# Kernel tuning notes

Measured on AMD Instinct MI355X. Metric: run time of the kernel, lower is better.

Reference implementation:

```python
import jax, jax.numpy as jnp
import numpy as np

NA, NB = 40000, 40000
D_IN, D_OUT, H, C = 256, 256, 8, 32  # C = D_OUT // H
E = 400000
N_MP = 3


def setup_inputs() -> dict:
    key = jax.random.key(0)
    ks = jax.random.split(key, 16)
    s = 1.0 / np.sqrt(D_IN)
    inp = {
        "x_A": jax.random.normal(ks[0], (NA, D_IN), jnp.float32),
        "x_B": jax.random.normal(ks[1], (NB, D_IN), jnp.float32),
        "edge_ab": jax.random.randint(ks[2], (2, E), 0, NB, jnp.int32),  # src in A, dst in B
        "edge_ba": jax.random.randint(ks[3], (2, E), 0, NA, jnp.int32),  # src in B, dst in A
        "edge_aa": jax.random.randint(ks[4], (2, E), 0, NA, jnp.int32),  # src in A, dst in A
        "W_A": jax.random.normal(ks[5], (D_IN, D_OUT), jnp.float32) * s,
        "b_A": jnp.zeros((D_OUT,), jnp.float32),
        "W_B": jax.random.normal(ks[6], (D_IN, D_OUT), jnp.float32) * s,
        "b_B": jnp.zeros((D_OUT,), jnp.float32),
        "attn_l": jax.random.normal(ks[7], (N_MP, H, C), jnp.float32) * 0.1,
        "attn_r": jax.random.normal(ks[8], (N_MP, H, C), jnp.float32) * 0.1,
        "rel_l_A": jax.random.normal(ks[9], (H, C), jnp.float32) * 0.1,
        "rel_r_A": jax.random.normal(ks[10], (H, C), jnp.float32) * 0.1,
        "rel_l_B": jax.random.normal(ks[11], (H, C), jnp.float32) * 0.1,
        "rel_r_B": jax.random.normal(ks[12], (H, C), jnp.float32) * 0.1,
    }
    return inp


def _leaky(x):
    return jax.nn.leaky_relu(x, negative_slope=0.2)


def _gat_relation(h_src, edge, a_l, a_r, n_dst):
    """GAT-style edge attention + segment softmax + scatter-add.
    h_src: [N_src,H,C], edge: [2,E], a_l: [N_src,H], a_r: [N_dst,H]."""
    src, dst = edge[0], edge[1]
    e = _leaky(a_l[src] + a_r[dst])                      # [E,H]
    m = jax.ops.segment_max(e, dst, num_segments=n_dst)  # [N_dst,H]
    ex = jnp.exp(e - m[dst])
    denom = jax.ops.segment_sum(ex, dst, num_segments=n_dst)
    alpha = ex / denom[dst]                              # softmax over in-neighbors
    msg = h_src[src] * alpha[:, :, None]                 # [E,H,C]
    return jax.ops.segment_sum(msg, dst, num_segments=n_dst)  # [N_dst,H,C]


def _beta_combine(h, rel_embs, rel_l, rel_r):
    """Relation-level attention (get_beta_weights) + weighted sum.
    h: [N,H,C], rel_embs: [N,H,R,C]."""
    bl = (h * rel_l).sum(-1)                                 # [N,H]
    br = (rel_embs * rel_r[None, :, None, :]).sum(-1)        # [N,H,R]
    beta = jax.nn.softmax(_leaky(bl[:, :, None] + br), axis=2)
    out = (rel_embs * beta[..., None]).sum(2)                # [N,H,C]
    return out.reshape(out.shape[0], H * C)


def reference(x_A, x_B, edge_ab, edge_ba, edge_aa, W_A, b_A, W_B, b_B,
              attn_l, attn_r, rel_l_A, rel_r_A, rel_l_B, rel_r_B):
    nA, nB = x_A.shape[0], x_B.shape[0]
    h_A = (x_A @ W_A + b_A).reshape(nA, H, C)
    h_B = (x_B @ W_B + b_B).reshape(nB, H, C)

    # per-metapath node attention scalars (get_alphas)
    # metapath 0: A->B, 1: B->A, 2: A->A
    al0 = (h_A * attn_l[0]).sum(-1); ar0 = (h_B * attn_r[0]).sum(-1)
    al1 = (h_B * attn_l[1]).sum(-1); ar1 = (h_A * attn_r[1]).sum(-1)
    al2 = (h_A * attn_l[2]).sum(-1); ar2 = (h_A * attn_r[2]).sum(-1)

    # aggregate per tail relation (agg_relation_neighbors); last slot = self
    rel_ba = _gat_relation(h_B, edge_ba, al1, ar1, nA)
    rel_aa = _gat_relation(h_A, edge_aa, al2, ar2, nA)
    emb_A = jnp.stack([rel_ba, rel_aa, h_A], axis=2)         # [NA,H,3,C]

    rel_ab = _gat_relation(h_A, edge_ab, al0, ar0, nB)
    emb_B = jnp.stack([rel_ab, h_B], axis=2)                 # [NB,H,2,C]

    out_A = jax.nn.relu(_beta_combine(h_A, emb_A, rel_l_A, rel_r_A))
    out_B = jax.nn.relu(_beta_combine(h_B, emb_B, rel_l_B, rel_r_B))
    return jnp.concatenate([out_A, out_B], axis=0)           # [NA+NB, D_OUT]
```

## Files before the change

### kernel.cpp

```cpp
#include <hip/hip_runtime.h>
#include <math.h>

#define NAn 40000
#define NBn 40000
#define DIN 256
#define DOUT 256
#define NH 8
#define NC 32
#define NE 400000
#define CAP 64

typedef __attribute__((ext_vector_type(8))) short short8;
typedef __attribute__((ext_vector_type(4))) float floatx4;

__device__ __forceinline__ float leaky(float x) { return x > 0.f ? x : 0.2f * x; }
__device__ __forceinline__ float dot4(float4 a, float4 b) {
  return a.x * b.x + a.y * b.y + a.z * b.z + a.w * b.w;
}
__device__ __forceinline__ unsigned bf16_rne_bits(float x) {
  unsigned u = __float_as_uint(x);
  unsigned r = u + 0x7fffu + ((u >> 16) & 1u);
  return r & 0xffff0000u;
}
__device__ __forceinline__ float4 bf4(uint2 u) {
  float4 f;
  f.x = __uint_as_float(u.x << 16);
  f.y = __uint_as_float(u.x & 0xffff0000u);
  f.z = __uint_as_float(u.y << 16);
  f.w = __uint_as_float(u.y & 0xffff0000u);
  return f;
}
__device__ __forceinline__ void bf8(uint4 u, float* f) {
  f[0] = __uint_as_float(u.x << 16);
  f[1] = __uint_as_float(u.x & 0xffff0000u);
  f[2] = __uint_as_float(u.y << 16);
  f[3] = __uint_as_float(u.y & 0xffff0000u);
  f[4] = __uint_as_float(u.z << 16);
  f[5] = __uint_as_float(u.z & 0xffff0000u);
  f[6] = __uint_as_float(u.w << 16);
  f[7] = __uint_as_float(u.w & 0xffff0000u);
}

__global__ void wswz(const float* __restrict__ WA, const float* __restrict__ WB,
                     short8* __restrict__ hiA, short8* __restrict__ hiB) {
  int t = blockIdx.x * blockDim.x + threadIdx.x;
  const float* W;
  short8* hi;
  if (t < 8192) {
    W = WA; hi = hiA;
  } else {
    t -= 8192;
    if (t >= 8192) return;
    W = WB; hi = hiB;
  }
  int kt = t >> 10, nt = (t >> 6) & 15, l = t & 63;
  int n = nt * 16 + (l & 15);
  int kb = kt * 32 + (l >> 4) * 8;
  short8 h8;
#pragma unroll
  for (int j = 0; j < 8; ++j) {
    float w = W[(size_t)(kb + j) * DOUT + n];
    h8[j] = (short)(bf16_rne_bits(w) >> 16);
  }
  hi[t] = h8;
}

__global__ __launch_bounds__(256) void gemm_mfma(
    const float* __restrict__ XA, const float* __restrict__ XB,
    const short8* __restrict__ WAhi, const short8* __restrict__ WBhi,
    const float* __restrict__ bA, const float* __restrict__ bB,
    unsigned* __restrict__ HAbf, unsigned* __restrict__ HBbf) {
  __shared__ short8 bfrag[2][1024];
  int blk = blockIdx.x;
  const float* X;
  const short8* Wh;
  const float* bias;
  unsigned* Hbf;
  if (blk < NAn / 64) {
    X = XA; Wh = WAhi; bias = bA; Hbf = HAbf;
  } else {
    blk -= NAn / 64;
    X = XB; Wh = WBhi; bias = bB; Hbf = HBbf;
  }
  const int tid = threadIdx.x;
  const int lane = tid & 63, wave = tid >> 6;
  const int row0 = blk * 64 + wave * 16;
  const int col16 = lane & 15, quad = lane >> 4;

  floatx4 acc[16];
#pragma unroll
  for (int i = 0; i < 16; ++i) acc[i] = (floatx4){0.f, 0.f, 0.f, 0.f};

  const float4* xp = (const float4*)(X + (size_t)(row0 + col16) * DIN) + quad * 2;

  uint4 pre[4];
  const uint4* wsrc = (const uint4*)Wh;
#pragma unroll
  for (int c = 0; c < 4; ++c) pre[c] = wsrc[c * 256 + tid];
  {
    uint4* d = (uint4*)&bfrag[0][0];
#pragma unroll
    for (int c = 0; c < 4; ++c) d[c * 256 + tid] = pre[c];
  }
  __syncthreads();

  for (int kt = 0; kt < 8; ++kt) {
    if (kt < 7) {
      const uint4* s = wsrc + (size_t)(kt + 1) * 1024;
#pragma unroll
      for (int c = 0; c < 4; ++c) pre[c] = s[c * 256 + tid];
    }
    float4 x0 = xp[kt * 8];
    float4 x1 = xp[kt * 8 + 1];
    float xv[8] = {x0.x, x0.y, x0.z, x0.w, x1.x, x1.y, x1.z, x1.w};
    short8 ahi, alo;
#pragma unroll
    for (int j = 0; j < 8; ++j) {
      unsigned hb = bf16_rne_bits(xv[j]);
      ahi[j] = (short)(hb >> 16);
      float rem = xv[j] - __uint_as_float(hb);
      alo[j] = (short)(bf16_rne_bits(rem) >> 16);
    }
    const short8* bp = &bfrag[kt & 1][0];
#pragma unroll
    for (int nt = 0; nt < 16; ++nt) {
      short8 bv = bp[nt * 64 + lane];
      acc[nt] = __builtin_amdgcn_mfma_f32_16x16x32_bf16(ahi, bv, acc[nt], 0, 0, 0);
      acc[nt] = __builtin_amdgcn_mfma_f32_16x16x32_bf16(alo, bv, acc[nt], 0, 0, 0);
    }
    if (kt < 7) {
      uint4* d = (uint4*)&bfrag[(kt + 1) & 1][0];
#pragma unroll
      for (int c = 0; c < 4; ++c) d[c * 256 + tid] = pre[c];
    }
    __syncthreads();
  }
#pragma unroll
  for (int nt = 0; nt < 16; ++nt) {
    float bcol = bias[nt * 16 + col16];
#pragma unroll
    for (int r = 0; r < 4; ++r) {
      int row = row0 + quad * 4 + r;
      float v = acc[nt][r] + bcol;
      float vp = __shfl_xor(v, 1);
      if ((lane & 1) == 0) {
        unsigned p = (bf16_rne_bits(v) >> 16) | bf16_rne_bits(vp);
        Hbf[(size_t)row * 128 + nt * 8 + (col16 >> 1)] = p;
      }
    }
  }
}

__global__ void alphas(const uint2* __restrict__ hAbf, const uint2* __restrict__ hBbf,
                       const float* __restrict__ attn_l, const float* __restrict__ attn_r,
                       float* __restrict__ al0, float* __restrict__ ar1,
                       float* __restrict__ al2, float* __restrict__ ar2,
                       float* __restrict__ ar0, float* __restrict__ al1) {
  int idx = blockIdx.x * blockDim.x + threadIdx.x;
  if (idx >= (NAn + NBn) * NH) return;
  bool isA = idx < NAn * NH;
  int k = isA ? idx : idx - NAn * NH;
  int head = k & 7;
  const uint2* h8 = (isA ? hAbf : hBbf) + (size_t)k * 8;
  if (isA) {
    const float4* l0 = (const float4*)(attn_l + 0 * DOUT + head * NC);
    const float4* r1 = (const float4*)(attn_r + 1 * DOUT + head * NC);
    const float4* l2 = (const float4*)(attn_l + 2 * DOUT + head * NC);
    const float4* r2 = (const float4*)(attn_r + 2 * DOUT + head * NC);
    float s0 = 0, s1 = 0, s2 = 0, s3 = 0;
#pragma unroll
    for (int q = 0; q < 8; ++q) {
      float4 hv = bf4(h8[q]);
      s0 += dot4(hv, l0[q]);
      s1 += dot4(hv, r1[q]);
      s2 += dot4(hv, l2[q]);
      s3 += dot4(hv, r2[q]);
    }
    al0[k] = s0;
    ar1[k] = s1;
    al2[k] = s2;
    ar2[k] = s3;
  } else {
    const float4* r0 = (const float4*)(attn_r + 0 * DOUT + head * NC);
    const float4* l1 = (const float4*)(attn_l + 1 * DOUT + head * NC);
    float s0 = 0, s1 = 0;
#pragma unroll
    for (int q = 0; q < 8; ++q) {
      float4 hv = bf4(h8[q]);
      s0 += dot4(hv, r0[q]);
      s1 += dot4(hv, l1[q]);
    }
    ar0[k] = s0;
    al1[k] = s1;
  }
}

__global__ void build_csr3(const int* __restrict__ e_ba, const int* __restrict__ e_aa,
                           const int* __restrict__ e_ab, int* __restrict__ cnt_ba,
                           int* __restrict__ cnt_aa, int* __restrict__ cnt_ab,
                           int* __restrict__ sl_ba, int* __restrict__ sl_aa,
                           int* __restrict__ sl_ab) {
  int i = blockIdx.x * blockDim.x + threadIdx.x;
  if (i >= 3 * NE) return;
  const int* e;
  int* cnt;
  int* sl;
  int k = i;
  if (i < NE) {
    e = e_ba; cnt = cnt_ba; sl = sl_ba;
  } else if (i < 2 * NE) {
    e = e_aa; cnt = cnt_aa; sl = sl_aa; k = i - NE;
  } else {
    e = e_ab; cnt = cnt_ab; sl = sl_ab; k = i - 2 * NE;
  }
  int src = e[k];
  int dst = e[NE + k];
  int pos = atomicAdd(&cnt[dst], 1);
  if (pos < CAP) sl[(size_t)dst * CAP + pos] = src;
}

__device__ __forceinline__ void gat2(int dst, int wave, int lane, int h, int sub, int head,
                                     const int* __restrict__ cnt,
                                     const int* __restrict__ slots,
                                     const float* __restrict__ al,
                                     const float* __restrict__ ar,
                                     const uint4* __restrict__ hbf,
                                     int lds_slot[4][64], float lds_ex[4][512],
                                     float acc[8]) {
#pragma unroll
  for (int k = 0; k < 8; ++k) acc[k] = 0.f;
  int deg = cnt[dst];
  if (deg > CAP) deg = CAP;
  if (deg == 0) return;
  __threadfence_block();
  if (lane < deg) {
    int s = slots[(size_t)dst * CAP + lane];
    lds_slot[wave][lane] = s;
    float4 a0 = *(const float4*)(al + (size_t)s * 8);
    float4 a1 = *(const float4*)(al + (size_t)s * 8 + 4);
    float4 r0 = *(const float4*)(ar + (size_t)dst * 8);
    float4 r1 = *(const float4*)(ar + (size_t)dst * 8 + 4);
    float* exq = &lds_ex[wave][lane * 8];
    exq[0] = __expf(leaky(a0.x + r0.x));
    exq[1] = __expf(leaky(a0.y + r0.y));
    exq[2] = __expf(leaky(a0.z + r0.z));
    exq[3] = __expf(leaky(a0.w + r0.w));
    exq[4] = __expf(leaky(a1.x + r1.x));
    exq[5] = __expf(leaky(a1.y + r1.y));
    exq[6] = __expf(leaky(a1.z + r1.z));
    exq[7] = __expf(leaky(a1.w + r1.w));
  }
  __threadfence_block();
  float den = 0.f;
  int iters = (deg + 1) >> 1;
  for (int it = 0; it < iters; ++it) {
    int j = it * 2 + h;
    if (j < deg) {
      int sj = lds_slot[wave][j];
      float w = lds_ex[wave][j * 8 + head];
      uint4 u = hbf[(size_t)sj * 32 + sub];
      den += w;
      float f[8];
      bf8(u, f);
#pragma unroll
      for (int k = 0; k < 8; ++k) acc[k] += w * f[k];
    }
  }
#pragma unroll
  for (int k = 0; k < 8; ++k) acc[k] += __shfl_xor(acc[k], 32);
  den += __shfl_xor(den, 32);
  float inv = 1.f / den;
#pragma unroll
  for (int k = 0; k < 8; ++k) acc[k] *= inv;
}

__global__ __launch_bounds__(256) void agg_combine(
    const int* __restrict__ cnt_ba, const int* __restrict__ sl_ba,
    const float* __restrict__ al1, const float* __restrict__ ar1,
    const int* __restrict__ cnt_aa, const int* __restrict__ sl_aa,
    const float* __restrict__ al2, const float* __restrict__ ar2,
    const int* __restrict__ cnt_ab, const int* __restrict__ sl_ab,
    const float* __restrict__ al0, const float* __restrict__ ar0,
    const uint4* __restrict__ hAbf, const uint4* __restrict__ hBbf,
    const float* __restrict__ rlA, const float* __restrict__ rrA,
    const float* __restrict__ rlB, const float* __restrict__ rrB,
    float* __restrict__ outp) {
  __shared__ int lds_slot[4][64];
  __shared__ float lds_ex[4][512];
  int wave = threadIdx.x >> 6, lane = threadIdx.x & 63;
  int h = lane >> 5, sub = lane & 31, head = sub >> 2;
  bool isA = blockIdx.x < (NAn / 4);
  int dst = (isA ? blockIdx.x : blockIdx.x - NAn / 4) * 4 + wave;
  float m0[8], hv[8], o[8];
  if (isA) {
    float m1[8];
    gat2(dst, wave, lane, h, sub, head, cnt_ba, sl_ba, al1, ar1, hBbf, lds_slot, lds_ex, m0);
    gat2(dst, wave, lane, h, sub, head, cnt_aa, sl_aa, al2, ar2, hAbf, lds_slot, lds_ex, m1);
    uint4 us = hAbf[(size_t)dst * 32 + sub];
    bf8(us, hv);
    const float4* rl4 = (const float4*)rlA;
    const float4* rr4 = (const float4*)rrA;
    float4 rl0 = rl4[sub * 2], rl1 = rl4[sub * 2 + 1];
    float4 rr0 = rr4[sub * 2], rr1 = rr4[sub * 2 + 1];
    float rl8[8] = {rl0.x, rl0.y, rl0.z, rl0.w, rl1.x, rl1.y, rl1.z, rl1.w};
    float rr8[8] = {rr0.x, rr0.y, rr0.z, rr0.w, rr1.x, rr1.y, rr1.z, rr1.w};
    float pbl = 0, p0 = 0, p1 = 0, p2 = 0;
#pragma unroll
    for (int k = 0; k < 8; ++k) {
      pbl += hv[k] * rl8[k];
      p0 += m0[k] * rr8[k];
      p1 += m1[k] * rr8[k];
      p2 += hv[k] * rr8[k];
    }
#pragma unroll
    for (int d = 1; d < 4; d <<= 1) {
      pbl += __shfl_xor(pbl, d);
      p0 += __shfl_xor(p0, d);
      p1 += __shfl_xor(p1, d);
      p2 += __shfl_xor(p2, d);
    }
    float b0 = leaky(pbl + p0), b1 = leaky(pbl + p1), b2 = leaky(pbl + p2);
    float mx = fmaxf(b0, fmaxf(b1, b2));
    float w0 = __expf(b0 - mx), w1 = __expf(b1 - mx), w2 = __expf(b2 - mx);
    float inv = 1.f / (w0 + w1 + w2);
    w0 *= inv; w1 *= inv; w2 *= inv;
#pragma unroll
    for (int k = 0; k < 8; ++k)
      o[k] = fmaxf(0.f, m0[k] * w0 + m1[k] * w1 + hv[k] * w2);
  } else {
    gat2(dst, wave, lane, h, sub, head, cnt_ab, sl_ab, al0, ar0, hAbf, lds_slot, lds_ex, m0);
    uint4 us = hBbf[(size_t)dst * 32 + sub];
    bf8(us, hv);
    const float4* rl4 = (const float4*)rlB;
    const float4* rr4 = (const float4*)rrB;
    float4 rl0 = rl4[sub * 2], rl1 = rl4[sub * 2 + 1];
    float4 rr0 = rr4[sub * 2], rr1 = rr4[sub * 2 + 1];
    float rl8[8] = {rl0.x, rl0.y, rl0.z, rl0.w, rl1.x, rl1.y, rl1.z, rl1.w};
    float rr8[8] = {rr0.x, rr0.y, rr0.z, rr0.w, rr1.x, rr1.y, rr1.z, rr1.w};
    float pbl = 0, p0 = 0, p1 = 0;
#pragma unroll
    for (int k = 0; k < 8; ++k) {
      pbl += hv[k] * rl8[k];
      p0 += m0[k] * rr8[k];
      p1 += hv[k] * rr8[k];
    }
#pragma unroll
    for (int d = 1; d < 4; d <<= 1) {
      pbl += __shfl_xor(pbl, d);
      p0 += __shfl_xor(p0, d);
      p1 += __shfl_xor(p1, d);
    }
    float b0 = leaky(pbl + p0), b1 = leaky(pbl + p1);
    float mx = fmaxf(b0, b1);
    float w0 = __expf(b0 - mx), w1 = __expf(b1 - mx);
    float inv = 1.f / (w0 + w1);
    w0 *= inv; w1 *= inv;
#pragma unroll
    for (int k = 0; k < 8; ++k) o[k] = fmaxf(0.f, m0[k] * w0 + hv[k] * w1);
  }
  float* orow = outp + (size_t)(isA ? dst : NAn + dst) * DOUT + sub * 8;
  if (h == 0) {
    *(float4*)orow = (float4){o[0], o[1], o[2], o[3]};
    *(float4*)(orow + 4) = (float4){o[4], o[5], o[6], o[7]};
  }
}

extern "C" void kernel_launch(void* const* d_in, const int* in_sizes, int n_in, void* d_out,
                              int out_size, void* d_ws, size_t ws_size, hipStream_t stream) {
  const float* xA = (const float*)d_in[0];
  const float* xB = (const float*)d_in[1];
  const int* e_ab = (const int*)d_in[2];
  const int* e_ba = (const int*)d_in[3];
  const int* e_aa = (const int*)d_in[4];
  const float* WA = (const float*)d_in[5];
  const float* bA = (const float*)d_in[6];
  const float* WB = (const float*)d_in[7];
  const float* bB = (const float*)d_in[8];
  const float* attn_l = (const float*)d_in[9];
  const float* attn_r = (const float*)d_in[10];
  const float* rlA = (const float*)d_in[11];
  const float* rrA = (const float*)d_in[12];
  const float* rlB = (const float*)d_in[13];
  const float* rrB = (const float*)d_in[14];
  float* out = (float*)d_out;

  char* p = (char*)d_ws;
  auto alloc = [&](size_t bytes) -> char* {
    char* r = p;
    p += (bytes + 255) & ~(size_t)255;
    return r;
  };
  unsigned* hAbf = (unsigned*)alloc((size_t)NAn * DOUT * 2);
  unsigned* hBbf = (unsigned*)alloc((size_t)NBn * DOUT * 2);
  float* al0 = (float*)alloc((size_t)NAn * NH * 4);
  float* ar1 = (float*)alloc((size_t)NAn * NH * 4);
  float* al2 = (float*)alloc((size_t)NAn * NH * 4);
  float* ar2 = (float*)alloc((size_t)NAn * NH * 4);
  float* ar0 = (float*)alloc((size_t)NBn * NH * 4);
  float* al1 = (float*)alloc((size_t)NBn * NH * 4);
  short8* WAhi = (short8*)alloc((size_t)8192 * 16);
  short8* WBhi = (short8*)alloc((size_t)8192 * 16);
  int* cnts = (int*)alloc((size_t)3 * NAn * 4);
  int* cnt_ba = cnts;
  int* cnt_aa = cnts + NAn;
  int* cnt_ab = cnts + 2 * NAn;
  int* slots_ba = (int*)alloc((size_t)NAn * CAP * 4);
  int* slots_aa = (int*)alloc((size_t)NAn * CAP * 4);
  int* slots_ab = (int*)alloc((size_t)NBn * CAP * 4);

  hipMemsetAsync(cnts, 0, (size_t)3 * NAn * 4, stream);

  wswz<<<64, 256, 0, stream>>>(WA, WB, WAhi, WBhi);
  build_csr3<<<(3 * NE + 255) / 256, 256, 0, stream>>>(e_ba, e_aa, e_ab, cnt_ba, cnt_aa,
                                                       cnt_ab, slots_ba, slots_aa, slots_ab);
  gemm_mfma<<<(NAn + NBn) / 64, 256, 0, stream>>>(xA, xB, WAhi, WBhi, bA, bB, hAbf, hBbf);
  alphas<<<((NAn + NBn) * NH + 255) / 256, 256, 0, stream>>>(
      (const uint2*)hAbf, (const uint2*)hBbf, attn_l, attn_r, al0, ar1, al2, ar2, ar0, al1);
  agg_combine<<<(NAn + NBn) / 4, 256, 0, stream>>>(
      cnt_ba, slots_ba, al1, ar1, cnt_aa, slots_aa, al2, ar2, cnt_ab, slots_ab, al0, ar0,
      (const uint4*)hAbf, (const uint4*)hBbf, rlA, rrA, rlB, rrB, out);
}
```

Baseline: 433.2 us.

## Split edge gather four ways with software prefetch and fold counter reset into swizzle

The aggregation kernel now has each wave process four edges at a time, with 16 lanes per edge each loading two 16-byte chunks. The next edge's row is prefetched while the current one accumulates, and setup for both relations is done up front with a single fence. This aims to raise memory-level parallelism in the gather-bound aggregation, and a launch-bounds occupancy hint is added. The separate memset of the degree counters is folded into the weight-swizzle kernel to drop one launch. The costs are more registers for the doubled accumulators and more cross-lane reductions.

```diff
diff --git a/kernel.cpp b/kernel.cpp
--- a/kernel.cpp
+++ b/kernel.cpp
@@ -42,18 +42,21 @@
 }
 
 __global__ void wswz(const float* __restrict__ WA, const float* __restrict__ WB,
-                     short8* __restrict__ hiA, short8* __restrict__ hiB) {
+                     short8* __restrict__ hiA, short8* __restrict__ hiB,
+                     int* __restrict__ cnts) {
   int t = blockIdx.x * blockDim.x + threadIdx.x;
+  for (int i = t; i < 3 * NAn; i += 16384) cnts[i] = 0;
   const float* W;
   short8* hi;
-  if (t < 8192) {
+  int tt = t;
+  if (tt < 8192) {
     W = WA; hi = hiA;
   } else {
-    t -= 8192;
-    if (t >= 8192) return;
+    tt -= 8192;
+    if (tt >= 8192) return;
     W = WB; hi = hiB;
   }
-  int kt = t >> 10, nt = (t >> 6) & 15, l = t & 63;
+  int kt = tt >> 10, nt = (tt >> 6) & 15, l = tt & 63;
   int n = nt * 16 + (l & 15);
   int kb = kt * 32 + (l >> 4) * 8;
   short8 h8;
@@ -62,7 +65,7 @@
     float w = W[(size_t)(kb + j) * DOUT + n];
     h8[j] = (short)(bf16_rne_bits(w) >> 16);
   }
-  hi[t] = h8;
+  hi[tt] = h8;
 }
 
 __global__ __launch_bounds__(256) void gemm_mfma(
@@ -219,62 +222,77 @@
   if (pos < CAP) sl[(size_t)dst * CAP + pos] = src;
 }
 
-__device__ __forceinline__ void gat2(int dst, int wave, int lane, int h, int sub, int head,
-                                     const int* __restrict__ cnt,
-                                     const int* __restrict__ slots,
-                                     const float* __restrict__ al,
-                                     const float* __restrict__ ar,
-                                     const uint4* __restrict__ hbf,
-                                     int lds_slot[4][64], float lds_ex[4][512],
-                                     float acc[8]) {
-#pragma unroll
-  for (int k = 0; k < 8; ++k) acc[k] = 0.f;
+__device__ __forceinline__ int setup_rel(int dst, int wave, int lane, int ridx,
+                                         const int* __restrict__ cnt,
+                                         const int* __restrict__ slots,
+                                         const float* __restrict__ al,
+                                         const float* __restrict__ ar,
+                                         int lds_slot[4][2][64],
+                                         float lds_ex[4][2][512]) {
   int deg = cnt[dst];
   if (deg > CAP) deg = CAP;
-  if (deg == 0) return;
-  __threadfence_block();
   if (lane < deg) {
     int s = slots[(size_t)dst * CAP + lane];
-    lds_slot[wave][lane] = s;
+    lds_slot[wave][ridx][lane] = s;
     float4 a0 = *(const float4*)(al + (size_t)s * 8);
     float4 a1 = *(const float4*)(al + (size_t)s * 8 + 4);
     float4 r0 = *(const float4*)(ar + (size_t)dst * 8);
     float4 r1 = *(const float4*)(ar + (size_t)dst * 8 + 4);
-    float* exq = &lds_ex[wave][lane * 8];
-    exq[0] = __expf(leaky(a0.x + r0.x));
-    exq[1] = __expf(leaky(a0.y + r0.y));
-    exq[2] = __expf(leaky(a0.z + r0.z));
-    exq[3] = __expf(leaky(a0.w + r0.w));
-    exq[4] = __expf(leaky(a1.x + r1.x));
-    exq[5] = __expf(leaky(a1.y + r1.y));
-    exq[6] = __expf(leaky(a1.z + r1.z));
-    exq[7] = __expf(leaky(a1.w + r1.w));
-  }
-  __threadfence_block();
-  float den = 0.f;
-  int iters = (deg + 1) >> 1;
-  for (int it = 0; it < iters; ++it) {
-    int j = it * 2 + h;
-    if (j < deg) {
-      int sj = lds_slot[wave][j];
-      float w = lds_ex[wave][j * 8 + head];
-      uint4 u = hbf[(size_t)sj * 32 + sub];
-      den += w;
-      float f[8];
-      bf8(u, f);
-#pragma unroll
-      for (int k = 0; k < 8; ++k) acc[k] += w * f[k];
-    }
-  }
-#pragma unroll
-  for (int k = 0; k < 8; ++k) acc[k] += __shfl_xor(acc[k], 32);
-  den += __shfl_xor(den, 32);
-  float inv = 1.f / den;
-#pragma unroll
-  for (int k = 0; k < 8; ++k) acc[k] *= inv;
-}
-
-__global__ __launch_bounds__(256) void agg_combine(
+    float4 e0, e1;
+    e0.x = __expf(leaky(a0.x + r0.x));
+    e0.y = __expf(leaky(a0.y + r0.y));
+    e0.z = __expf(leaky(a0.z + r0.z));
+    e0.w = __expf(leaky(a0.w + r0.w));
+    e1.x = __expf(leaky(a1.x + r1.x));
+    e1.y = __expf(leaky(a1.y + r1.y));
+    e1.z = __expf(leaky(a1.z + r1.z));
+    e1.w = __expf(leaky(a1.w + r1.w));
+    *(float4*)&lds_ex[wave][ridx][lane * 8] = e0;
+    *(float4*)&lds_ex[wave][ridx][lane * 8 + 4] = e1;
+  }
+  return deg;
+}
+
+__device__ __forceinline__ void edges4(int deg, int wave, int ridx, int h4, int hd0,
+                                       int s16, const uint4* __restrict__ hbf,
+                                       int lds_slot[4][2][64], float lds_ex[4][2][512],
+                                       float acc0[8], float acc1[8], float& den0,
+                                       float& den1) {
+  int j = h4;
+  if (j >= deg) return;
+  int sj = lds_slot[wave][ridx][j];
+  float w0 = lds_ex[wave][ridx][j * 8 + hd0];
+  float w1 = lds_ex[wave][ridx][j * 8 + hd0 + 4];
+  const uint4* bp = hbf + (size_t)sj * 32;
+  uint4 u0 = bp[s16];
+  uint4 u1 = bp[s16 + 16];
+  while (true) {
+    uint4 cu0 = u0, cu1 = u1;
+    float cw0 = w0, cw1 = w1;
+    int jn = j + 4;
+    if (jn < deg) {
+      int sn = lds_slot[wave][ridx][jn];
+      w0 = lds_ex[wave][ridx][jn * 8 + hd0];
+      w1 = lds_ex[wave][ridx][jn * 8 + hd0 + 4];
+      const uint4* bn = hbf + (size_t)sn * 32;
+      u0 = bn[s16];
+      u1 = bn[s16 + 16];
+    }
+    den0 += cw0;
+    den1 += cw1;
+    float f0[8], f1[8];
+    bf8(cu0, f0);
+    bf8(cu1, f1);
+#pragma unroll
+    for (int k = 0; k < 8; ++k) acc0[k] += cw0 * f0[k];
+#pragma unroll
+    for (int k = 0; k < 8; ++k) acc1[k] += cw1 * f1[k];
+    j = jn;
+    if (j >= deg) break;
+  }
+}
+
+__global__ __launch_bounds__(256, 4) void agg_combine(
     const int* __restrict__ cnt_ba, const int* __restrict__ sl_ba,
     const float* __restrict__ al1, const float* __restrict__ ar1,
     const int* __restrict__ cnt_aa, const int* __restrict__ sl_aa,
@@ -285,83 +303,166 @@
     const float* __restrict__ rlA, const float* __restrict__ rrA,
     const float* __restrict__ rlB, const float* __restrict__ rrB,
     float* __restrict__ outp) {
-  __shared__ int lds_slot[4][64];
-  __shared__ float lds_ex[4][512];
+  __shared__ int lds_slot[4][2][64];
+  __shared__ float lds_ex[4][2][512];
   int wave = threadIdx.x >> 6, lane = threadIdx.x & 63;
-  int h = lane >> 5, sub = lane & 31, head = sub >> 2;
+  int h4 = lane >> 4, s16 = lane & 15;
+  int hd0 = s16 >> 2;
+  int c0 = s16, c1 = s16 + 16;
   bool isA = blockIdx.x < (NAn / 4);
   int dst = (isA ? blockIdx.x : blockIdx.x - NAn / 4) * 4 + wave;
-  float m0[8], hv[8], o[8];
+
   if (isA) {
-    float m1[8];
-    gat2(dst, wave, lane, h, sub, head, cnt_ba, sl_ba, al1, ar1, hBbf, lds_slot, lds_ex, m0);
-    gat2(dst, wave, lane, h, sub, head, cnt_aa, sl_aa, al2, ar2, hAbf, lds_slot, lds_ex, m1);
-    uint4 us = hAbf[(size_t)dst * 32 + sub];
-    bf8(us, hv);
+    int deg0 = setup_rel(dst, wave, lane, 0, cnt_ba, sl_ba, al1, ar1, lds_slot, lds_ex);
+    int deg1 = setup_rel(dst, wave, lane, 1, cnt_aa, sl_aa, al2, ar2, lds_slot, lds_ex);
+    uint4 us0 = hAbf[(size_t)dst * 32 + c0];
+    uint4 us1 = hAbf[(size_t)dst * 32 + c1];
+    __threadfence_block();
+    float m00[8], m01[8], m10[8], m11[8];
+    float den00 = 0.f, den01 = 0.f, den10 = 0.f, den11 = 0.f;
+#pragma unroll
+    for (int k = 0; k < 8; ++k) { m00[k] = 0.f; m01[k] = 0.f; m10[k] = 0.f; m11[k] = 0.f; }
+    edges4(deg0, wave, 0, h4, hd0, s16, hBbf, lds_slot, lds_ex, m00, m01, den00, den01);
+    edges4(deg1, wave, 1, h4, hd0, s16, hAbf, lds_slot, lds_ex, m10, m11, den10, den11);
+#pragma unroll
+    for (int k = 0; k < 8; ++k) {
+      m00[k] += __shfl_xor(m00[k], 16); m00[k] += __shfl_xor(m00[k], 32);
+      m01[k] += __shfl_xor(m01[k], 16); m01[k] += __shfl_xor(m01[k], 32);
+      m10[k] += __shfl_xor(m10[k], 16); m10[k] += __shfl_xor(m10[k], 32);
+      m11[k] += __shfl_xor(m11[k], 16); m11[k] += __shfl_xor(m11[k], 32);
+    }
+    den00 += __shfl_xor(den00, 16); den00 += __shfl_xor(den00, 32);
+    den01 += __shfl_xor(den01, 16); den01 += __shfl_xor(den01, 32);
+    den10 += __shfl_xor(den10, 16); den10 += __shfl_xor(den10, 32);
+    den11 += __shfl_xor(den11, 16); den11 += __shfl_xor(den11, 32);
+    if (deg0 > 0) {
+      float i0 = 1.f / den00, i1 = 1.f / den01;
+#pragma unroll
+      for (int k = 0; k < 8; ++k) { m00[k] *= i0; m01[k] *= i1; }
+    }
+    if (deg1 > 0) {
+      float i0 = 1.f / den10, i1 = 1.f / den11;
+#pragma unroll
+      for (int k = 0; k < 8; ++k) { m10[k] *= i0; m11[k] *= i1; }
+    }
+    float hv0[8], hv1[8];
+    bf8(us0, hv0);
+    bf8(us1, hv1);
     const float4* rl4 = (const float4*)rlA;
     const float4* rr4 = (const float4*)rrA;
-    float4 rl0 = rl4[sub * 2], rl1 = rl4[sub * 2 + 1];
-    float4 rr0 = rr4[sub * 2], rr1 = rr4[sub * 2 + 1];
-    float rl8[8] = {rl0.x, rl0.y, rl0.z, rl0.w, rl1.x, rl1.y, rl1.z, rl1.w};
-    float rr8[8] = {rr0.x, rr0.y, rr0.z, rr0.w, rr1.x, rr1.y, rr1.z, rr1.w};
-    float pbl = 0, p0 = 0, p1 = 0, p2 = 0;
+    float4 la = rl4[c0 * 2], lb = rl4[c0 * 2 + 1], lc = rl4[c1 * 2], ld = rl4[c1 * 2 + 1];
+    float4 ra = rr4[c0 * 2], rb = rr4[c0 * 2 + 1], rc = rr4[c1 * 2], rd = rr4[c1 * 2 + 1];
+    float rl0[8] = {la.x, la.y, la.z, la.w, lb.x, lb.y, lb.z, lb.w};
+    float rl1[8] = {lc.x, lc.y, lc.z, lc.w, ld.x, ld.y, ld.z, ld.w};
+    float rr0[8] = {ra.x, ra.y, ra.z, ra.w, rb.x, rb.y, rb.z, rb.w};
+    float rr1[8] = {rc.x, rc.y, rc.z, rc.w, rd.x, rd.y, rd.z, rd.w};
+    float pbl0 = 0, pbl1 = 0, q00 = 0, q01 = 0, q10 = 0, q11 = 0, q20 = 0, q21 = 0;
 #pragma unroll
     for (int k = 0; k < 8; ++k) {
-      pbl += hv[k] * rl8[k];
-      p0 += m0[k] * rr8[k];
-      p1 += m1[k] * rr8[k];
-      p2 += hv[k] * rr8[k];
+      pbl0 += hv0[k] * rl0[k]; pbl1 += hv1[k] * rl1[k];
+      q00 += m00[k] * rr0[k];  q01 += m01[k] * rr1[k];
+      q10 += m10[k] * rr0[k];  q11 += m11[k] * rr1[k];
+      q20 += hv0[k] * rr0[k];  q21 += hv1[k] * rr1[k];
     }
 #pragma unroll
     for (int d = 1; d < 4; d <<= 1) {
-      pbl += __shfl_xor(pbl, d);
-      p0 += __shfl_xor(p0, d);
-      p1 += __shfl_xor(p1, d);
-      p2 += __shfl_xor(p2, d);
-    }
-    float b0 = leaky(pbl + p0), b1 = leaky(pbl + p1), b2 = leaky(pbl + p2);
+      pbl0 += __shfl_xor(pbl0, d); pbl1 += __shfl_xor(pbl1, d);
+      q00 += __shfl_xor(q00, d);   q01 += __shfl_xor(q01, d);
+      q10 += __shfl_xor(q10, d);   q11 += __shfl_xor(q11, d);
+      q20 += __shfl_xor(q20, d);   q21 += __shfl_xor(q21, d);
+    }
+    float b0 = leaky(pbl0 + q00), b1 = leaky(pbl0 + q10), b2 = leaky(pbl0 + q20);
     float mx = fmaxf(b0, fmaxf(b1, b2));
     float w0 = __expf(b0 - mx), w1 = __expf(b1 - mx), w2 = __expf(b2 - mx);
     float inv = 1.f / (w0 + w1 + w2);
     w0 *= inv; w1 *= inv; w2 *= inv;
-#pragma unroll
-    for (int k = 0; k < 8; ++k)
-      o[k] = fmaxf(0.f, m0[k] * w0 + m1[k] * w1 + hv[k] * w2);
+    float d0 = leaky(pbl1 + q01), d1 = leaky(pbl1 + q11), d2 = leaky(pbl1 + q21);
+    float mx1 = fmaxf(d0, fmaxf(d1, d2));
+    float v0 = __expf(d0 - mx1), v1 = __expf(d1 - mx1), v2 = __expf(d2 - mx1);
+    float inv1 = 1.f / (v0 + v1 + v2);
+    v0 *= inv1; v1 *= inv1; v2 *= inv1;
+    if (h4 == 0) {
+      float o0[8], o1[8];
+#pragma unroll
+      for (int k = 0; k < 8; ++k) {
+        o0[k] = fmaxf(0.f, m00[k] * w0 + m10[k] * w1 + hv0[k] * w2);
+        o1[k] = fmaxf(0.f, m01[k] * v0 + m11[k] * v1 + hv1[k] * v2);
+      }
+      float* orow = outp + (size_t)dst * DOUT;
+      *(float4*)(orow + c0 * 8) = (float4){o0[0], o0[1], o0[2], o0[3]};
+      *(float4*)(orow + c0 * 8 + 4) = (float4){o0[4], o0[5], o0[6], o0[7]};
+      *(float4*)(orow + c1 * 8) = (float4){o1[0], o1[1], o1[2], o1[3]};
+      *(float4*)(orow + c1 * 8 + 4) = (float4){o1[4], o1[5], o1[6], o1[7]};
+    }
   } else {
-    gat2(dst, wave, lane, h, sub, head, cnt_ab, sl_ab, al0, ar0, hAbf, lds_slot, lds_ex, m0);
-    uint4 us = hBbf[(size_t)dst * 32 + sub];
-    bf8(us, hv);
+    int deg = setup_rel(dst, wave, lane, 0, cnt_ab, sl_ab, al0, ar0, lds_slot, lds_ex);
+    uint4 us0 = hBbf[(size_t)dst * 32 + c0];
+    uint4 us1 = hBbf[(size_t)dst * 32 + c1];
+    __threadfence_block();
+    float m00[8], m01[8];
+    float den00 = 0.f, den01 = 0.f;
+#pragma unroll
+    for (int k = 0; k < 8; ++k) { m00[k] = 0.f; m01[k] = 0.f; }
+    edges4(deg, wave, 0, h4, hd0, s16, hAbf, lds_slot, lds_ex, m00, m01, den00, den01);
+#pragma unroll
+    for (int k = 0; k < 8; ++k) {
+      m00[k] += __shfl_xor(m00[k], 16); m00[k] += __shfl_xor(m00[k], 32);
+      m01[k] += __shfl_xor(m01[k], 16); m01[k] += __shfl_xor(m01[k], 32);
+    }
+    den00 += __shfl_xor(den00, 16); den00 += __shfl_xor(den00, 32);
+    den01 += __shfl_xor(den01, 16); den01 += __shfl_xor(den01, 32);
+    if (deg > 0) {
+      float i0 = 1.f / den00, i1 = 1.f / den01;
+#pragma unroll
+      for (int k = 0; k < 8; ++k) { m00[k] *= i0; m01[k] *= i1; }
+    }
+    float hv0[8], hv1[8];
+    bf8(us0, hv0);
+    bf8(us1, hv1);
     const float4* rl4 = (const float4*)rlB;
     const float4* rr4 = (const float4*)rrB;
-    float4 rl0 = rl4[sub * 2], rl1 = rl4[sub * 2 + 1];
-    float4 rr0 = rr4[sub * 2], rr1 = rr4[sub * 2 + 1];
-    float rl8[8] = {rl0.x, rl0.y, rl0.z, rl0.w, rl1.x, rl1.y, rl1.z, rl1.w};
-    float rr8[8] = {rr0.x, rr0.y, rr0.z, rr0.w, rr1.x, rr1.y, rr1.z, rr1.w};
-    float pbl = 0, p0 = 0, p1 = 0;
+    float4 la = rl4[c0 * 2], lb = rl4[c0 * 2 + 1], lc = rl4[c1 * 2], ld = rl4[c1 * 2 + 1];
+    float4 ra = rr4[c0 * 2], rb = rr4[c0 * 2 + 1], rc = rr4[c1 * 2], rd = rr4[c1 * 2 + 1];
+    float rl0[8] = {la.x, la.y, la.z, la.w, lb.x, lb.y, lb.z, lb.w};
+    float rl1[8] = {lc.x, lc.y, lc.z, lc.w, ld.x, ld.y, ld.z, ld.w};
+    float rr0[8] = {ra.x, ra.y, ra.z, ra.w, rb.x, rb.y, rb.z, rb.w};
+    float rr1[8] = {rc.x, rc.y, rc.z, rc.w, rd.x, rd.y, rd.z, rd.w};
+    float pbl0 = 0, pbl1 = 0, q00 = 0, q01 = 0, q20 = 0, q21 = 0;
 #pragma unroll
     for (int k = 0; k < 8; ++k) {
-      pbl += hv[k] * rl8[k];
-      p0 += m0[k] * rr8[k];
-      p1 += hv[k] * rr8[k];
+      pbl0 += hv0[k] * rl0[k]; pbl1 += hv1[k] * rl1[k];
+      q00 += m00[k] * rr0[k];  q01 += m01[k] * rr1[k];
+      q20 += hv0[k] * rr0[k];  q21 += hv1[k] * rr1[k];
     }
 #pragma unroll
     for (int d = 1; d < 4; d <<= 1) {
-      pbl += __shfl_xor(pbl, d);
-      p0 += __shfl_xor(p0, d);
-      p1 += __shfl_xor(p1, d);
-    }
-    float b0 = leaky(pbl + p0), b1 = leaky(pbl + p1);
+      pbl0 += __shfl_xor(pbl0, d); pbl1 += __shfl_xor(pbl1, d);
+      q00 += __shfl_xor(q00, d);   q01 += __shfl_xor(q01, d);
+      q20 += __shfl_xor(q20, d);   q21 += __shfl_xor(q21, d);
+    }
+    float b0 = leaky(pbl0 + q00), b1 = leaky(pbl0 + q20);
     float mx = fmaxf(b0, b1);
     float w0 = __expf(b0 - mx), w1 = __expf(b1 - mx);
     float inv = 1.f / (w0 + w1);
     w0 *= inv; w1 *= inv;
-#pragma unroll
-    for (int k = 0; k < 8; ++k) o[k] = fmaxf(0.f, m0[k] * w0 + hv[k] * w1);
-  }
-  float* orow = outp + (size_t)(isA ? dst : NAn + dst) * DOUT + sub * 8;
-  if (h == 0) {
-    *(float4*)orow = (float4){o[0], o[1], o[2], o[3]};
-    *(float4*)(orow + 4) = (float4){o[4], o[5], o[6], o[7]};
+    float d0 = leaky(pbl1 + q01), d1 = leaky(pbl1 + q21);
+    float mx1 = fmaxf(d0, d1);
+    float v0 = __expf(d0 - mx1), v1 = __expf(d1 - mx1);
+    float inv1 = 1.f / (v0 + v1);
+    v0 *= inv1; v1 *= inv1;
+    if (h4 == 0) {
+      float o0[8], o1[8];
+#pragma unroll
+      for (int k = 0; k < 8; ++k) {
+        o0[k] = fmaxf(0.f, m00[k] * w0 + hv0[k] * w1);
+        o1[k] = fmaxf(0.f, m01[k] * v0 + hv1[k] * v1);
+      }
+      float* orow = outp + (size_t)(NAn + dst) * DOUT;
+      *(float4*)(orow + c0 * 8) = (float4){o0[0], o0[1], o0[2], o0[3]};
+      *(float4*)(orow + c0 * 8 + 4) = (float4){o0[4], o0[5], o0[6], o0[7]};
+      *(float4*)(orow + c1 * 8) = (float4){o1[0], o1[1], o1[2], o1[3]};
+      *(float4*)(orow + c1 * 8 + 4) = (float4){o1[4], o1[5], o1[6], o1[7]};
+    }
   }
 }
 
@@ -408,9 +509,7 @@
   int* slots_aa = (int*)alloc((size_t)NAn * CAP * 4);
   int* slots_ab = (int*)alloc((size_t)NBn * CAP * 4);
 
-  hipMemsetAsync(cnts, 0, (size_t)3 * NAn * 4, stream);
-
-  wswz<<<64, 256, 0, stream>>>(WA, WB, WAhi, WBhi);
+  wswz<<<64, 256, 0, stream>>>(WA, WB, WAhi, WBhi, cnts);
   build_csr3<<<(3 * NE + 255) / 256, 256, 0, stream>>>(e_ba, e_aa, e_ab, cnt_ba, cnt_aa,
                                                        cnt_ab, slots_ba, slots_aa, slots_ab);
   gemm_mfma<<<(NAn + NBn) / 64, 256, 0, stream>>>(xA, xB, WAhi, WBhi, bA, bB, hAbf, hBbf);
```

Result: slower. 475.0 us (+9.7%).

## Fuse attention-scalar computation into GEMM epilogue and fold counter memset into weight swizzle

Applied to the files above, without the earlier changes.

The GEMM epilogue now also writes the bf16 outputs to LDS, then computes the per-node, per-head attention dot products there. This removes the separate alphas kernel and its re-read of the projected features from global memory. The count-array memset moves into the weight-swizzle kernel to save one launch, and the CSR build uses nontemporal loads and stores for edges and slots. The cost is extra epilogue work and LDS traffic in the GEMM.

```diff
diff --git a/kernel.cpp b/kernel.cpp
--- a/kernel.cpp
+++ b/kernel.cpp
@@ -14,21 +14,10 @@
 typedef __attribute__((ext_vector_type(4))) float floatx4;
 
 __device__ __forceinline__ float leaky(float x) { return x > 0.f ? x : 0.2f * x; }
-__device__ __forceinline__ float dot4(float4 a, float4 b) {
-  return a.x * b.x + a.y * b.y + a.z * b.z + a.w * b.w;
-}
 __device__ __forceinline__ unsigned bf16_rne_bits(float x) {
   unsigned u = __float_as_uint(x);
   unsigned r = u + 0x7fffu + ((u >> 16) & 1u);
   return r & 0xffff0000u;
-}
-__device__ __forceinline__ float4 bf4(uint2 u) {
-  float4 f;
-  f.x = __uint_as_float(u.x << 16);
-  f.y = __uint_as_float(u.x & 0xffff0000u);
-  f.z = __uint_as_float(u.y << 16);
-  f.w = __uint_as_float(u.y & 0xffff0000u);
-  return f;
 }
 __device__ __forceinline__ void bf8(uint4 u, float* f) {
   f[0] = __uint_as_float(u.x << 16);
@@ -42,18 +31,21 @@
 }
 
 __global__ void wswz(const float* __restrict__ WA, const float* __restrict__ WB,
-                     short8* __restrict__ hiA, short8* __restrict__ hiB) {
+                     short8* __restrict__ hiA, short8* __restrict__ hiB,
+                     int* __restrict__ cnts) {
   int t = blockIdx.x * blockDim.x + threadIdx.x;
+  for (int i = t; i < 3 * NAn; i += 16384) cnts[i] = 0;
   const float* W;
   short8* hi;
-  if (t < 8192) {
+  int tt = t;
+  if (tt < 8192) {
     W = WA; hi = hiA;
   } else {
-    t -= 8192;
-    if (t >= 8192) return;
+    tt -= 8192;
+    if (tt >= 8192) return;
     W = WB; hi = hiB;
   }
-  int kt = t >> 10, nt = (t >> 6) & 15, l = t & 63;
+  int kt = tt >> 10, nt = (tt >> 6) & 15, l = tt & 63;
   int n = nt * 16 + (l & 15);
   int kb = kt * 32 + (l >> 4) * 8;
   short8 h8;
@@ -62,21 +54,26 @@
     float w = W[(size_t)(kb + j) * DOUT + n];
     h8[j] = (short)(bf16_rne_bits(w) >> 16);
   }
-  hi[t] = h8;
+  hi[tt] = h8;
 }
 
 __global__ __launch_bounds__(256) void gemm_mfma(
     const float* __restrict__ XA, const float* __restrict__ XB,
     const short8* __restrict__ WAhi, const short8* __restrict__ WBhi,
     const float* __restrict__ bA, const float* __restrict__ bB,
-    unsigned* __restrict__ HAbf, unsigned* __restrict__ HBbf) {
+    const float* __restrict__ attn_l, const float* __restrict__ attn_r,
+    unsigned* __restrict__ HAbf, unsigned* __restrict__ HBbf,
+    float* __restrict__ al0, float* __restrict__ ar1,
+    float* __restrict__ al2, float* __restrict__ ar2,
+    float* __restrict__ ar0, float* __restrict__ al1) {
   __shared__ short8 bfrag[2][1024];
   int blk = blockIdx.x;
+  const bool isA = blk < (NAn / 64);
   const float* X;
   const short8* Wh;
   const float* bias;
   unsigned* Hbf;
-  if (blk < NAn / 64) {
+  if (isA) {
     X = XA; Wh = WAhi; bias = bA; Hbf = HAbf;
   } else {
     blk -= NAn / 64;
@@ -135,63 +132,58 @@
     }
     __syncthreads();
   }
+  unsigned* lds_u = (unsigned*)&bfrag[0][0];
 #pragma unroll
   for (int nt = 0; nt < 16; ++nt) {
     float bcol = bias[nt * 16 + col16];
 #pragma unroll
     for (int r = 0; r < 4; ++r) {
-      int row = row0 + quad * 4 + r;
+      int rl = wave * 16 + quad * 4 + r;
       float v = acc[nt][r] + bcol;
       float vp = __shfl_xor(v, 1);
       if ((lane & 1) == 0) {
         unsigned p = (bf16_rne_bits(v) >> 16) | bf16_rne_bits(vp);
-        Hbf[(size_t)row * 128 + nt * 8 + (col16 >> 1)] = p;
+        Hbf[(size_t)(blk * 64 + rl) * 128 + nt * 8 + (col16 >> 1)] = p;
+        lds_u[rl * 128 + nt * 8 + (col16 >> 1)] = p;
       }
     }
   }
-}
-
-__global__ void alphas(const uint2* __restrict__ hAbf, const uint2* __restrict__ hBbf,
-                       const float* __restrict__ attn_l, const float* __restrict__ attn_r,
-                       float* __restrict__ al0, float* __restrict__ ar1,
-                       float* __restrict__ al2, float* __restrict__ ar2,
-                       float* __restrict__ ar0, float* __restrict__ al1) {
-  int idx = blockIdx.x * blockDim.x + threadIdx.x;
-  if (idx >= (NAn + NBn) * NH) return;
-  bool isA = idx < NAn * NH;
-  int k = isA ? idx : idx - NAn * NH;
-  int head = k & 7;
-  const uint2* h8 = (isA ? hAbf : hBbf) + (size_t)k * 8;
-  if (isA) {
-    const float4* l0 = (const float4*)(attn_l + 0 * DOUT + head * NC);
-    const float4* r1 = (const float4*)(attn_r + 1 * DOUT + head * NC);
-    const float4* l2 = (const float4*)(attn_l + 2 * DOUT + head * NC);
-    const float4* r2 = (const float4*)(attn_r + 2 * DOUT + head * NC);
-    float s0 = 0, s1 = 0, s2 = 0, s3 = 0;
-#pragma unroll
-    for (int q = 0; q < 8; ++q) {
-      float4 hv = bf4(h8[q]);
-      s0 += dot4(hv, l0[q]);
-      s1 += dot4(hv, r1[q]);
-      s2 += dot4(hv, l2[q]);
-      s3 += dot4(hv, r2[q]);
-    }
-    al0[k] = s0;
-    ar1[k] = s1;
-    al2[k] = s2;
-    ar2[k] = s3;
-  } else {
-    const float4* r0 = (const float4*)(attn_r + 0 * DOUT + head * NC);
-    const float4* l1 = (const float4*)(attn_l + 1 * DOUT + head * NC);
-    float s0 = 0, s1 = 0;
-#pragma unroll
-    for (int q = 0; q < 8; ++q) {
-      float4 hv = bf4(h8[q]);
-      s0 += dot4(hv, r0[q]);
-      s1 += dot4(hv, l1[q]);
-    }
-    ar0[k] = s0;
-    al1[k] = s1;
+  __syncthreads();
+#pragma unroll
+  for (int t = 0; t < 2; ++t) {
+    int task = tid + t * 256;
+    int rl = task >> 3, head = task & 7;
+    int node = blk * 64 + rl;
+    int k = node * 8 + head;
+    float f[32];
+    const uint4* lp = (const uint4*)(lds_u + rl * 128 + head * 16);
+#pragma unroll
+    for (int q = 0; q < 4; ++q) bf8(lp[q], &f[q * 8]);
+    if (isA) {
+      const float* l0 = attn_l + 0 * DOUT + head * NC;
+      const float* r1 = attn_r + 1 * DOUT + head * NC;
+      const float* l2 = attn_l + 2 * DOUT + head * NC;
+      const float* r2 = attn_r + 2 * DOUT + head * NC;
+      float s0 = 0, s1 = 0, s2 = 0, s3 = 0;
+#pragma unroll
+      for (int c = 0; c < 32; ++c) {
+        s0 += f[c] * l0[c];
+        s1 += f[c] * r1[c];
+        s2 += f[c] * l2[c];
+        s3 += f[c] * r2[c];
+      }
+      al0[k] = s0; ar1[k] = s1; al2[k] = s2; ar2[k] = s3;
+    } else {
+      const float* r0 = attn_r + 0 * DOUT + head * NC;
+      const float* l1 = attn_l + 1 * DOUT + head * NC;
+      float s0 = 0, s1 = 0;
+#pragma unroll
+      for (int c = 0; c < 32; ++c) {
+        s0 += f[c] * r0[c];
+        s1 += f[c] * l1[c];
+      }
+      ar0[k] = s0; al1[k] = s1;
+    }
   }
 }
 
@@ -213,10 +205,10 @@
   } else {
     e = e_ab; cnt = cnt_ab; sl = sl_ab; k = i - 2 * NE;
   }
-  int src = e[k];
-  int dst = e[NE + k];
+  int src = __builtin_nontemporal_load(&e[k]);
+  int dst = __builtin_nontemporal_load(&e[NE + k]);
   int pos = atomicAdd(&cnt[dst], 1);
-  if (pos < CAP) sl[(size_t)dst * CAP + pos] = src;
+  if (pos < CAP) __builtin_nontemporal_store(src, &sl[(size_t)dst * CAP + pos]);
 }
 
 __device__ __forceinline__ void gat2(int dst, int wave, int lane, int h, int sub, int head,
@@ -408,14 +400,12 @@
   int* slots_aa = (int*)alloc((size_t)NAn * CAP * 4);
   int* slots_ab = (int*)alloc((size_t)NBn * CAP * 4);
 
-  hipMemsetAsync(cnts, 0, (size_t)3 * NAn * 4, stream);
-
-  wswz<<<64, 256, 0, stream>>>(WA, WB, WAhi, WBhi);
+  wswz<<<64, 256, 0, stream>>>(WA, WB, WAhi, WBhi, cnts);
   build_csr3<<<(3 * NE + 255) / 256, 256, 0, stream>>>(e_ba, e_aa, e_ab, cnt_ba, cnt_aa,
                                                        cnt_ab, slots_ba, slots_aa, slots_ab);
-  gemm_mfma<<<(NAn + NBn) / 64, 256, 0, stream>>>(xA, xB, WAhi, WBhi, bA, bB, hAbf, hBbf);
-  alphas<<<((NAn + NBn) * NH + 255) / 256, 256, 0, stream>>>(
-      (const uint2*)hAbf, (const uint2*)hBbf, attn_l, attn_r, al0, ar1, al2, ar2, ar0, al1);
+  gemm_mfma<<<(NAn + NBn) / 64, 256, 0, stream>>>(xA, xB, WAhi, WBhi, bA, bB, attn_l,
+                                                  attn_r, hAbf, hBbf, al0, ar1, al2, ar2,
+                                                  ar0, al1);
   agg_combine<<<(NAn + NBn) / 4, 256, 0, stream>>>(
       cnt_ba, slots_ba, al1, ar1, cnt_aa, slots_aa, al2, ar2, cnt_ab, slots_ab, al0, ar0,
       (const uint4*)hAbf, (const uint4*)hBbf, rlA, rrA, rlB, rrB, out);
```

Measured after the change: 474.6 us. 1.1x slower.
